# Kernel optimization log

Measured on AMD Instinct MI355X. Metric: run time of the kernel, lower is better.

The kernel has to match this reference:

```python
import jax, jax.numpy as jnp
import numpy as np
import math

N_HEAD = 16

def _rope_tables(seq, dh, dtype):
    inv_freq = 1.0 / (10000.0 ** (jnp.arange(0, dh, 2, dtype=jnp.float32) / dh))
    angle = jnp.arange(seq, dtype=jnp.float32)[:, None] * inv_freq[None, :]  # [S, dh/2]
    sin = jnp.repeat(jnp.sin(angle), 2, axis=-1).astype(dtype)  # [S, dh]
    cos = jnp.repeat(jnp.cos(angle), 2, axis=-1).astype(dtype)
    return sin, cos

def _rotate_half(x):
    x_even = x[..., ::2]
    x_odd = x[..., 1::2]
    return jnp.stack([-x_odd, x_even], axis=-1).reshape(x.shape)

def _apply_rope(x, sin, cos):
    # x: [B, H, S, dh]; sin/cos: [S, dh]
    return x * cos[None, None] + _rotate_half(x) * sin[None, None]

def setup_inputs() -> dict:
    key = jax.random.key(0)
    ks = jax.random.split(key, 9)
    B, S, D = 2, 2048, 2048
    scale = 1.0 / math.sqrt(D)
    x = jax.random.normal(ks[0], (B, S, D), dtype=jnp.float32)
    wq = jax.random.normal(ks[1], (D, D), dtype=jnp.float32) * scale
    wk = jax.random.normal(ks[2], (D, D), dtype=jnp.float32) * scale
    wv = jax.random.normal(ks[3], (D, D), dtype=jnp.float32) * scale
    wo = jax.random.normal(ks[4], (D, D), dtype=jnp.float32) * scale
    bq = jnp.zeros((D,), jnp.float32)
    bk = jnp.zeros((D,), jnp.float32)
    bv = jnp.zeros((D,), jnp.float32)
    bo = jnp.zeros((D,), jnp.float32)
    # causal mask: True = masked (strict upper triangle)
    mask = jnp.triu(jnp.ones((S, S), dtype=bool), k=1)[None, None]  # [1,1,S,S]
    return {"x": x, "wq": wq, "bq": bq, "wk": wk, "bk": bk, "wv": wv, "bv": bv,
            "wo": wo, "bo": bo, "mask": mask}

def reference(x, wq, bq, wk, bk, wv, bv, wo, bo, mask):
    B, S, D = x.shape
    H = N_HEAD
    dh = D // H
    # projections (torch Linear: x @ W.T + b)
    q = (x @ wq.T + bq).reshape(B, S, H, dh).transpose(0, 2, 1, 3)  # [B,H,S,dh]
    k = (x @ wk.T + bk).reshape(B, S, H, dh).transpose(0, 2, 1, 3)
    v = (x @ wv.T + bv).reshape(B, S, H, dh).transpose(0, 2, 1, 3)
    sin, cos = _rope_tables(S, dh, x.dtype)
    q = _apply_rope(q, sin, cos)
    k = _apply_rope(k, sin, cos)
    scores = jnp.einsum('bhqd,bhkd->bhqk', q, k) / math.sqrt(dh)
    scores = jnp.where(mask, -jnp.inf, scores)
    attn = jax.nn.softmax(scores, axis=-1)
    attn = jnp.nan_to_num(attn, nan=0.0)
    out = jnp.einsum('bhqk,bhkd->bhqd', attn, v)  # [B,H,S,dh]
    out = out.transpose(0, 2, 1, 3).reshape(B, S, D)
    return out @ wo.T + bo
```

## Files before the change

kernel.cpp:

```cpp
#include <hip/hip_runtime.h>
#include <math.h>


typedef _Float16 half8 __attribute__((ext_vector_type(8)));
typedef _Float16 half4v __attribute__((ext_vector_type(4)));
typedef float f32x4 __attribute__((ext_vector_type(4)));

__device__ __forceinline__ void gl_lds16(const void* g, void* l) {
  __builtin_amdgcn_global_load_lds(
      (const __attribute__((address_space(1))) unsigned int*)g,
      (__attribute__((address_space(3))) unsigned int*)l, 16, 0, 0);
}

__global__ void cast_f32_f16(const float* __restrict__ src, _Float16* __restrict__ dst, int n4) {
  int i = blockIdx.x * blockDim.x + threadIdx.x;
  if (i >= n4) return;
  float4 v = reinterpret_cast<const float4*>(src)[i];
  half4v o;
  o[0] = (_Float16)v.x; o[1] = (_Float16)v.y; o[2] = (_Float16)v.z; o[3] = (_Float16)v.w;
  reinterpret_cast<half4v*>(dst)[i] = o;
}

__global__ void cast_w(const float* __restrict__ w0, const float* __restrict__ w1,
                       const float* __restrict__ w2, const float* __restrict__ w3,
                       _Float16* __restrict__ wdst) {
  const float* s = blockIdx.y == 0 ? w0 : blockIdx.y == 1 ? w1 : blockIdx.y == 2 ? w2 : w3;
  int i = blockIdx.x * blockDim.x + threadIdx.x;
  float4 v = reinterpret_cast<const float4*>(s)[i];
  half4v o;
  o[0] = (_Float16)v.x; o[1] = (_Float16)v.y; o[2] = (_Float16)v.z; o[3] = (_Float16)v.w;
  reinterpret_cast<half4v*>(wdst)[(size_t)blockIdx.y * 1048576 + i] = o;
}

template <bool OUT_F32>
__global__ __launch_bounds__(256, 2) void gemm_bt(
    const _Float16* __restrict__ A,
    const _Float16* __restrict__ B,
    const float* __restrict__ b0, const float* __restrict__ b1,
    const float* __restrict__ b2,
    void* __restrict__ Cout,
    int M, int N, int K) {
  __shared__ _Float16 As[2][4096];
  __shared__ _Float16 Bs[2][4096];
  const int bm = blockIdx.y * 128, bn = blockIdx.x * 128;
  const int tid = threadIdx.x;
  const int wave = tid >> 6, lane = tid & 63;
  const int quad = lane >> 4, l16 = lane & 15;
  const int hh = wave >> 1, gg = wave & 1;

  const _Float16* gsrc[4];
  int lofs[4];
#pragma unroll
  for (int p = 0; p < 4; ++p) {
    int c = ((p & 1) * 256 + tid) & 511;
    int cl16 = c & 15, cqd = (c >> 4) & 3, ci = (c >> 6) & 3, ch = c >> 8;
    int grow = ch * 64 + ci * 16 + cl16;
    int gcol = cqd * 8;
    gsrc[p] = (p < 2 ? A + (size_t)(bm + grow) * K : B + (size_t)(bn + grow) * K) + gcol;
    lofs[p] = c * 8;
  }

  f32x4 acc[4][4];
#pragma unroll
  for (int i = 0; i < 4; ++i)
#pragma unroll
    for (int n = 0; n < 4; ++n) acc[i][n] = f32x4{0.f, 0.f, 0.f, 0.f};

#pragma unroll
  for (int p = 0; p < 4; ++p)
    gl_lds16(gsrc[p], (p < 2 ? &As[0][lofs[p]] : &Bs[0][lofs[p]]));

  const int nit = K >> 5;
  for (int it = 0; it < nit; ++it) {
    __syncthreads();
    const int cur = it & 1;
    if (it + 1 < nit) {
      const int nxt = cur ^ 1, ko = (it + 1) * 32;
#pragma unroll
      for (int p = 0; p < 4; ++p)
        gl_lds16(gsrc[p] + ko, (p < 2 ? &As[nxt][lofs[p]] : &Bs[nxt][lofs[p]]));
    }
    half8 af[4], bf[4];
#pragma unroll
    for (int i = 0; i < 4; ++i)
      af[i] = *reinterpret_cast<const half8*>(&As[cur][((hh * 4 + i) * 4 + quad) * 128 + l16 * 8]);
#pragma unroll
    for (int n = 0; n < 4; ++n)
      bf[n] = *reinterpret_cast<const half8*>(&Bs[cur][((gg * 4 + n) * 4 + quad) * 128 + l16 * 8]);
#pragma unroll
    for (int i = 0; i < 4; ++i)
#pragma unroll
      for (int n = 0; n < 4; ++n)
        acc[i][n] = __builtin_amdgcn_mfma_f32_16x16x32_f16(af[i], bf[n], acc[i][n], 0, 0, 0);
  }

  const int wm = hh * 64, wn = gg * 64;
#pragma unroll
  for (int n = 0; n < 4; ++n) {
    const int gc = bn + wn + n * 16 + l16;
    const float* bp = (gc < 2048) ? b0 : (gc < 4096 ? b1 : b2);
    const float bz = bp[gc & 2047];
#pragma unroll
    for (int i = 0; i < 4; ++i) {
#pragma unroll
      for (int r = 0; r < 4; ++r) {
        const int gr = bm + wm + i * 16 + quad * 4 + r;
        float v = acc[i][n][r] + bz;
        if (OUT_F32)
          reinterpret_cast<float*>(Cout)[(size_t)gr * N + gc] = v;
        else
          reinterpret_cast<_Float16*>(Cout)[(size_t)gr * N + gc] = (_Float16)v;
      }
    }
  }
}

__global__ void rope_inplace(_Float16* __restrict__ qkv, int ngroups) {
  int idx = blockIdx.x * blockDim.x + threadIdx.x;
  if (idx >= ngroups) return;
  int m = idx >> 8;
  int g = idx & 255;
  int s = m & 2047;
  const float scale = 0.088388347648318447f;
  size_t base = (size_t)m * 6144 + g * 8;
  half8 qv = *reinterpret_cast<const half8*>(qkv + base);
  half8 kv = *reinterpret_cast<const half8*>(qkv + base + 2048);
  half8 qo, ko;
#pragma unroll
  for (int j = 0; j < 4; ++j) {
    int i = (g * 4 + j) & 63;
    float ang = (float)s * exp2f(-0.2076205059304601f * (float)i);
    float sn, cs;
    __sincosf(ang, &sn, &cs);
    float e = (float)qv[j * 2], o = (float)qv[j * 2 + 1];
    qo[j * 2]     = (_Float16)((e * cs - o * sn) * scale);
    qo[j * 2 + 1] = (_Float16)((o * cs + e * sn) * scale);
    e = (float)kv[j * 2]; o = (float)kv[j * 2 + 1];
    ko[j * 2]     = (_Float16)(e * cs - o * sn);
    ko[j * 2 + 1] = (_Float16)(o * cs + e * sn);
  }
  *reinterpret_cast<half8*>(qkv + base) = qo;
  *reinterpret_cast<half8*>(qkv + base + 2048) = ko;
}

__global__ __launch_bounds__(256) void transpose_v(const _Float16* __restrict__ qkv,
                                                   _Float16* __restrict__ vt) {
  __shared__ _Float16 t[64][72];
  const int s0 = blockIdx.x * 64;
  const int d0 = blockIdx.y * 64;
  const int bh = blockIdx.z;
  const int b = bh >> 4, h = bh & 15;
  const int tid = threadIdx.x;
#pragma unroll
  for (int p = 0; p < 2; ++p) {
    int chunk = p * 256 + tid;
    int r = chunk >> 3, c8 = (chunk & 7) * 8;
    *reinterpret_cast<half8*>(&t[r][c8]) = *reinterpret_cast<const half8*>(
        &qkv[(size_t)(b * 2048 + s0 + r) * 6144 + 4096 + h * 128 + d0 + c8]);
  }
  __syncthreads();
#pragma unroll
  for (int p = 0; p < 2; ++p) {
    int chunk = p * 256 + tid;
    int dr = chunk >> 3, c8 = (chunk & 7) * 8;
    half8 o;
#pragma unroll
    for (int j = 0; j < 8; ++j) o[j] = t[c8 + j][dr];
    *reinterpret_cast<half8*>(&vt[(size_t)(bh * 128 + d0 + dr) * 2048 + s0 + c8]) = o;
  }
}

__global__ __launch_bounds__(256, 2) void attn_kernel(
    const _Float16* __restrict__ QKV,
    const _Float16* __restrict__ VT,
    _Float16* __restrict__ ctx) {
  constexpr int LD = 6144, S = 2048;
  __shared__ _Float16 Ks[2][8192];
  __shared__ _Float16 Vs[2][8192];
  __shared__ _Float16 P[4][16][80];
  const int bid = blockIdx.x;
  const int bh = bid & 31;
  const int qt = 31 - (bid >> 5);
  const int b = bh >> 4, h = bh & 15;
  const int tid = threadIdx.x;
  const int wv = tid >> 6, lane = tid & 63;
  const int quad = lane >> 4, l16 = lane & 15;
  const int q0 = qt * 64 + wv * 16;

  const _Float16* qp = QKV + (size_t)(b * S + q0 + l16) * LD + h * 128;
  half8 aq[4];
#pragma unroll
  for (int ks = 0; ks < 4; ++ks)
    aq[ks] = *reinterpret_cast<const half8*>(qp + ks * 32 + quad * 8);

  const _Float16* gk[4];
  const _Float16* gv[4];
  int lofs[4];
#pragma unroll
  for (int p = 0; p < 4; ++p) {
    int c = p * 256 + tid;
    int cl16 = c & 15, cqd = (c >> 4) & 3;
    int cks = (c >> 6) & 3, cf = c >> 8;
    gk[p] = QKV + (size_t)(b * S + cf * 16 + cl16) * LD + 2048 + h * 128 + cks * 32 + cqd * 8;
    int ckv = (c >> 6) & 1, ct = c >> 7;
    gv[p] = VT + (size_t)(bh * 128 + ct * 16 + cl16) * S + ckv * 32 + cqd * 8;
    lofs[p] = c * 8;
  }

  f32x4 acc[8];
#pragma unroll
  for (int t = 0; t < 8; ++t) acc[t] = f32x4{0.f, 0.f, 0.f, 0.f};
  f32x4 lacc = f32x4{0.f, 0.f, 0.f, 0.f};
  float m_i[4];
#pragma unroll
  for (int r = 0; r < 4; ++r) m_i[r] = -INFINITY;

  half8 ones;
#pragma unroll
  for (int j = 0; j < 8; ++j) ones[j] = (_Float16)1.0f;

#pragma unroll
  for (int p = 0; p < 4; ++p) gl_lds16(gk[p], &Ks[0][lofs[p]]);
#pragma unroll
  for (int p = 0; p < 4; ++p) gl_lds16(gv[p], &Vs[0][lofs[p]]);

  for (int j = 0; j <= qt; ++j) {
    __syncthreads();
    const int cur = j & 1;
    if (j < qt) {
      const size_t ko = (size_t)(j + 1) * 64 * LD;
      const int vo = (j + 1) * 64;
#pragma unroll
      for (int p = 0; p < 4; ++p) gl_lds16(gk[p] + ko, &Ks[cur ^ 1][lofs[p]]);
#pragma unroll
      for (int p = 0; p < 4; ++p) gl_lds16(gv[p] + vo, &Vs[cur ^ 1][lofs[p]]);
    }
    f32x4 sf[4];
#pragma unroll
    for (int f = 0; f < 4; ++f) sf[f] = f32x4{0.f, 0.f, 0.f, 0.f};
#pragma unroll
    for (int f = 0; f < 4; ++f)
#pragma unroll
      for (int ks = 0; ks < 4; ++ks) {
        half8 bk = *reinterpret_cast<const half8*>(&Ks[cur][((f * 4 + ks) * 4 + quad) * 128 + l16 * 8]);
        sf[f] = __builtin_amdgcn_mfma_f32_16x16x32_f16(aq[ks], bk, sf[f], 0, 0, 0);
      }
    if (j == qt) {
      const int key0 = j * 64;
#pragma unroll
      for (int f = 0; f < 4; ++f) {
        const int key = key0 + f * 16 + l16;
#pragma unroll
        for (int r = 0; r < 4; ++r) {
          const int row = q0 + quad * 4 + r;
          sf[f][r] = (key <= row) ? sf[f][r] : -1e30f;
        }
      }
    }
    float alpha[4];
#pragma unroll
    for (int r = 0; r < 4; ++r) {
      float tm = fmaxf(fmaxf(sf[0][r], sf[1][r]), fmaxf(sf[2][r], sf[3][r]));
      tm = fmaxf(tm, __shfl_xor(tm, 1));
      tm = fmaxf(tm, __shfl_xor(tm, 2));
      tm = fmaxf(tm, __shfl_xor(tm, 4));
      tm = fmaxf(tm, __shfl_xor(tm, 8));
      const float mn = fmaxf(m_i[r], tm);
      alpha[r] = __expf(m_i[r] - mn);
      m_i[r] = mn;
    }
#pragma unroll
    for (int f = 0; f < 4; ++f)
#pragma unroll
      for (int r = 0; r < 4; ++r)
        P[wv][quad * 4 + r][f * 16 + l16] = (_Float16)__expf(sf[f][r] - m_i[r]);
    half8 pa0 = *reinterpret_cast<const half8*>(&P[wv][l16][quad * 8]);
    half8 pa1 = *reinterpret_cast<const half8*>(&P[wv][l16][32 + quad * 8]);
#pragma unroll
    for (int t = 0; t < 8; ++t)
#pragma unroll
      for (int r = 0; r < 4; ++r) acc[t][r] *= alpha[r];
#pragma unroll
    for (int r = 0; r < 4; ++r) lacc[r] *= alpha[r];
#pragma unroll
    for (int t = 0; t < 8; ++t) {
      half8 bv0 = *reinterpret_cast<const half8*>(&Vs[cur][((t * 2 + 0) * 4 + quad) * 128 + l16 * 8]);
      half8 bv1 = *reinterpret_cast<const half8*>(&Vs[cur][((t * 2 + 1) * 4 + quad) * 128 + l16 * 8]);
      acc[t] = __builtin_amdgcn_mfma_f32_16x16x32_f16(pa0, bv0, acc[t], 0, 0, 0);
      acc[t] = __builtin_amdgcn_mfma_f32_16x16x32_f16(pa1, bv1, acc[t], 0, 0, 0);
    }
    lacc = __builtin_amdgcn_mfma_f32_16x16x32_f16(pa0, ones, lacc, 0, 0, 0);
    lacc = __builtin_amdgcn_mfma_f32_16x16x32_f16(pa1, ones, lacc, 0, 0, 0);
  }

  float inv[4];
#pragma unroll
  for (int r = 0; r < 4; ++r) inv[r] = 1.0f / lacc[r];
#pragma unroll
  for (int t = 0; t < 8; ++t)
#pragma unroll
    for (int r = 0; r < 4; ++r)
      ctx[(size_t)(b * S + q0 + quad * 4 + r) * 2048 + h * 128 + t * 16 + l16] =
          (_Float16)(acc[t][r] * inv[r]);
}

extern "C" void kernel_launch(void* const* d_in, const int* in_sizes, int n_in,
                              void* d_out, int out_size, void* d_ws, size_t ws_size,
                              hipStream_t stream) {
  const float* x  = (const float*)d_in[0];
  const float* wq = (const float*)d_in[1];
  const float* bq = (const float*)d_in[2];
  const float* wk = (const float*)d_in[3];
  const float* bk = (const float*)d_in[4];
  const float* wv = (const float*)d_in[5];
  const float* bv = (const float*)d_in[6];
  const float* wo = (const float*)d_in[7];
  const float* bo = (const float*)d_in[8];

  _Float16* W      = (_Float16*)d_ws;
  _Float16* xh     = W;
  _Float16* wqkvh  = xh + 8388608;
  _Float16* woh    = wqkvh + 12582912;
  _Float16* qkvlin = woh + 4194304;
  _Float16* vT     = xh;
  _Float16* ctx    = wqkvh;

  cast_f32_f16<<<8192, 256, 0, stream>>>(x, xh, 2097152);
  cast_w<<<dim3(4096, 4), 256, 0, stream>>>(wq, wk, wv, wo, wqkvh);

  gemm_bt<false><<<dim3(48, 32), 256, 0, stream>>>(xh, wqkvh, bq, bk, bv, qkvlin,
                                                   4096, 6144, 2048);

  rope_inplace<<<4096, 256, 0, stream>>>(qkvlin, 1048576);
  transpose_v<<<dim3(32, 2, 32), 256, 0, stream>>>(qkvlin, vT);
  attn_kernel<<<1024, 256, 0, stream>>>(qkvlin, vT, ctx);

  gemm_bt<true><<<dim3(16, 32), 256, 0, stream>>>(ctx, woh, bo, bo, bo, (float*)d_out,
                                                  4096, 2048, 2048);
}
```

Measured before the change: 515.0 us.

## Replace 128x128 GEMM with 256x256 tiled, XOR-swizzled, phase-interleaved pipelined kernel

Rewrites the projection GEMM to use 256x256 output tiles with 512 threads, K-steps of 64, an XOR-swizzled LDS layout, and staged global-to-LDS prefetch split into four phases interleaved with MFMA blocks, using s_setprio and explicit vmcnt waits. The goal is higher arithmetic intensity per loaded byte, fewer LDS bank conflicts and better overlap of loads with matrix math. In exchange it uses 128KB of LDS per block and more accumulator registers. The output projection launches only 128 blocks, which may underfill the GPU's 256 CUs.

```diff
diff --git a/kernel.cpp b/kernel.cpp
--- a/kernel.cpp
+++ b/kernel.cpp
@@ -33,79 +33,154 @@
 }
 
 template <bool OUT_F32>
-__global__ __launch_bounds__(256, 2) void gemm_bt(
+__global__ __launch_bounds__(512, 2) void gemm_bt256(
     const _Float16* __restrict__ A,
     const _Float16* __restrict__ B,
     const float* __restrict__ b0, const float* __restrict__ b1,
     const float* __restrict__ b2,
     void* __restrict__ Cout,
     int M, int N, int K) {
-  __shared__ _Float16 As[2][4096];
-  __shared__ _Float16 Bs[2][4096];
-  const int bm = blockIdx.y * 128, bn = blockIdx.x * 128;
+  __shared__ _Float16 As[2][16384];
+  __shared__ _Float16 Bs[2][16384];
+  const int bm = blockIdx.y * 256, bn = blockIdx.x * 256;
   const int tid = threadIdx.x;
   const int wave = tid >> 6, lane = tid & 63;
   const int quad = lane >> 4, l16 = lane & 15;
-  const int hh = wave >> 1, gg = wave & 1;
-
-  const _Float16* gsrc[4];
-  int lofs[4];
-#pragma unroll
-  for (int p = 0; p < 4; ++p) {
-    int c = ((p & 1) * 256 + tid) & 511;
-    int cl16 = c & 15, cqd = (c >> 4) & 3, ci = (c >> 6) & 3, ch = c >> 8;
-    int grow = ch * 64 + ci * 16 + cl16;
-    int gcol = cqd * 8;
-    gsrc[p] = (p < 2 ? A + (size_t)(bm + grow) * K : B + (size_t)(bn + grow) * K) + gcol;
-    lofs[p] = c * 8;
-  }
-
-  f32x4 acc[4][4];
-#pragma unroll
-  for (int i = 0; i < 4; ++i)
-#pragma unroll
-    for (int n = 0; n < 4; ++n) acc[i][n] = f32x4{0.f, 0.f, 0.f, 0.f};
-
-#pragma unroll
-  for (int p = 0; p < 4; ++p)
-    gl_lds16(gsrc[p], (p < 2 ? &As[0][lofs[p]] : &Bs[0][lofs[p]]));
-
-  const int nit = K >> 5;
-  for (int it = 0; it < nit; ++it) {
-    __syncthreads();
-    const int cur = it & 1;
-    if (it + 1 < nit) {
-      const int nxt = cur ^ 1, ko = (it + 1) * 32;
-#pragma unroll
-      for (int p = 0; p < 4; ++p)
-        gl_lds16(gsrc[p] + ko, (p < 2 ? &As[nxt][lofs[p]] : &Bs[nxt][lofs[p]]));
-    }
-    half8 af[4], bf[4];
+  const int wm = (wave >> 2) * 128, wn = (wave & 3) * 64;
+
+  const int srow = tid >> 3;
+  const int sslot = (tid & 7) ^ (srow & 7);
+  const _Float16* Ag = A + (size_t)(bm + srow) * K + sslot * 8;
+  const _Float16* Bg = B + (size_t)(bn + srow) * K + sslot * 8;
+
+#define STAGE_A(buf, h, c, kt)                                      \
+  gl_lds16(Ag + (size_t)((h) * 128 + (c) * 64) * K + (kt) * 64,     \
+           &As[buf][(h) * 8192 + (c) * 4096 + tid * 8])
+#define STAGE_B(buf, h, c, kt)                                      \
+  gl_lds16(Bg + (size_t)((h) * 128 + (c) * 64) * K + (kt) * 64,     \
+           &Bs[buf][(h) * 8192 + (c) * 4096 + tid * 8])
+
+  const int axor = l16 & 7;
+  const int sl0 = ((0 + quad) ^ axor) * 8;
+  const int sl1 = ((4 + quad) ^ axor) * 8;
+  const int aoff = (wm + l16) * 64;
+  const int boff = (wn + l16) * 64;
+
+#define RD_A(i, kk) \
+  (*reinterpret_cast<const half8*>(&As[cur][aoff + (i) * 1024 + ((kk) ? sl1 : sl0)]))
+#define RD_B(j, kk) \
+  (*reinterpret_cast<const half8*>(&Bs[cur][boff + (j) * 1024 + ((kk) ? sl1 : sl0)]))
+
+  f32x4 acc[8][4];
+#pragma unroll
+  for (int i = 0; i < 8; ++i)
+#pragma unroll
+    for (int j = 0; j < 4; ++j) acc[i][j] = f32x4{0.f, 0.f, 0.f, 0.f};
+
+  half8 a[4][2], b[4][2];
+  const int NT = K >> 6;
+
+  STAGE_A(0, 0, 0, 0); STAGE_A(0, 0, 1, 0);
+  STAGE_A(0, 1, 0, 0); STAGE_A(0, 1, 1, 0);
+  STAGE_B(0, 0, 0, 0); STAGE_B(0, 0, 1, 0);
+  STAGE_B(0, 1, 0, 0); STAGE_B(0, 1, 1, 0);
+  if (NT > 1) {
+    STAGE_A(1, 0, 0, 1); STAGE_A(1, 0, 1, 1);
+    asm volatile("s_waitcnt vmcnt(2)");
+  } else {
+    asm volatile("s_waitcnt vmcnt(0)");
+  }
+  __builtin_amdgcn_s_barrier();
+
+  for (int t = 0; t < NT; ++t) {
+    const int cur = t & 1, nxt = cur ^ 1;
+    const bool pf = (t + 1 < NT);
+    const bool pf2 = (t + 2 < NT);
+
+#pragma unroll
+    for (int i = 0; i < 4; ++i) {
+      a[i][0] = RD_A(i, 0); a[i][1] = RD_A(i, 1);
+    }
+#pragma unroll
+    for (int j = 0; j < 2; ++j) {
+      b[j][0] = RD_B(j, 0); b[j][1] = RD_B(j, 1);
+    }
+    if (pf) { STAGE_A(nxt, 1, 0, t + 1); STAGE_A(nxt, 1, 1, t + 1); }
+    __builtin_amdgcn_s_barrier();
+    __builtin_amdgcn_s_setprio(1);
 #pragma unroll
     for (int i = 0; i < 4; ++i)
-      af[i] = *reinterpret_cast<const half8*>(&As[cur][((hh * 4 + i) * 4 + quad) * 128 + l16 * 8]);
-#pragma unroll
-    for (int n = 0; n < 4; ++n)
-      bf[n] = *reinterpret_cast<const half8*>(&Bs[cur][((gg * 4 + n) * 4 + quad) * 128 + l16 * 8]);
+#pragma unroll
+      for (int j = 0; j < 2; ++j) {
+        acc[i][j] = __builtin_amdgcn_mfma_f32_16x16x32_f16(a[i][0], b[j][0], acc[i][j], 0, 0, 0);
+        acc[i][j] = __builtin_amdgcn_mfma_f32_16x16x32_f16(a[i][1], b[j][1], acc[i][j], 0, 0, 0);
+      }
+    __builtin_amdgcn_s_setprio(0);
+    __builtin_amdgcn_s_barrier();
+
+#pragma unroll
+    for (int j = 2; j < 4; ++j) {
+      b[j][0] = RD_B(j, 0); b[j][1] = RD_B(j, 1);
+    }
+    if (pf) { STAGE_B(nxt, 0, 0, t + 1); STAGE_B(nxt, 0, 1, t + 1); }
+    __builtin_amdgcn_s_barrier();
+    __builtin_amdgcn_s_setprio(1);
 #pragma unroll
     for (int i = 0; i < 4; ++i)
 #pragma unroll
-      for (int n = 0; n < 4; ++n)
-        acc[i][n] = __builtin_amdgcn_mfma_f32_16x16x32_f16(af[i], bf[n], acc[i][n], 0, 0, 0);
-  }
-
-  const int wm = hh * 64, wn = gg * 64;
-#pragma unroll
-  for (int n = 0; n < 4; ++n) {
-    const int gc = bn + wn + n * 16 + l16;
+      for (int j = 2; j < 4; ++j) {
+        acc[i][j] = __builtin_amdgcn_mfma_f32_16x16x32_f16(a[i][0], b[j][0], acc[i][j], 0, 0, 0);
+        acc[i][j] = __builtin_amdgcn_mfma_f32_16x16x32_f16(a[i][1], b[j][1], acc[i][j], 0, 0, 0);
+      }
+    __builtin_amdgcn_s_setprio(0);
+    __builtin_amdgcn_s_barrier();
+
+#pragma unroll
+    for (int i = 0; i < 4; ++i) {
+      a[i][0] = RD_A(i + 4, 0); a[i][1] = RD_A(i + 4, 1);
+    }
+    if (pf) { STAGE_B(nxt, 1, 0, t + 1); STAGE_B(nxt, 1, 1, t + 1); }
+    __builtin_amdgcn_s_barrier();
+    __builtin_amdgcn_s_setprio(1);
+#pragma unroll
+    for (int i = 0; i < 4; ++i)
+#pragma unroll
+      for (int j = 0; j < 2; ++j) {
+        acc[i + 4][j] = __builtin_amdgcn_mfma_f32_16x16x32_f16(a[i][0], b[j][0], acc[i + 4][j], 0, 0, 0);
+        acc[i + 4][j] = __builtin_amdgcn_mfma_f32_16x16x32_f16(a[i][1], b[j][1], acc[i + 4][j], 0, 0, 0);
+      }
+    __builtin_amdgcn_s_setprio(0);
+    __builtin_amdgcn_s_barrier();
+
+    if (pf2) { STAGE_A(cur, 0, 0, t + 2); STAGE_A(cur, 0, 1, t + 2); }
+    __builtin_amdgcn_s_barrier();
+    __builtin_amdgcn_s_setprio(1);
+#pragma unroll
+    for (int i = 0; i < 4; ++i)
+#pragma unroll
+      for (int j = 2; j < 4; ++j) {
+        acc[i + 4][j] = __builtin_amdgcn_mfma_f32_16x16x32_f16(a[i][0], b[j][0], acc[i + 4][j], 0, 0, 0);
+        acc[i + 4][j] = __builtin_amdgcn_mfma_f32_16x16x32_f16(a[i][1], b[j][1], acc[i + 4][j], 0, 0, 0);
+      }
+    __builtin_amdgcn_s_setprio(0);
+    if (pf2)
+      asm volatile("s_waitcnt vmcnt(2)");
+    else
+      asm volatile("s_waitcnt vmcnt(0)");
+    __builtin_amdgcn_s_barrier();
+  }
+
+#pragma unroll
+  for (int j = 0; j < 4; ++j) {
+    const int gc = bn + wn + j * 16 + l16;
     const float* bp = (gc < 2048) ? b0 : (gc < 4096 ? b1 : b2);
     const float bz = bp[gc & 2047];
 #pragma unroll
-    for (int i = 0; i < 4; ++i) {
+    for (int i = 0; i < 8; ++i) {
 #pragma unroll
       for (int r = 0; r < 4; ++r) {
         const int gr = bm + wm + i * 16 + quad * 4 + r;
-        float v = acc[i][n][r] + bz;
+        float v = acc[i][j][r] + bz;
         if (OUT_F32)
           reinterpret_cast<float*>(Cout)[(size_t)gr * N + gc] = v;
         else
@@ -113,6 +188,10 @@
       }
     }
   }
+#undef STAGE_A
+#undef STAGE_B
+#undef RD_A
+#undef RD_B
 }
 
 __global__ void rope_inplace(_Float16* __restrict__ qkv, int ngroups) {
@@ -328,13 +407,13 @@
   cast_f32_f16<<<8192, 256, 0, stream>>>(x, xh, 2097152);
   cast_w<<<dim3(4096, 4), 256, 0, stream>>>(wq, wk, wv, wo, wqkvh);
 
-  gemm_bt<false><<<dim3(48, 32), 256, 0, stream>>>(xh, wqkvh, bq, bk, bv, qkvlin,
-                                                   4096, 6144, 2048);
+  gemm_bt256<false><<<dim3(24, 16), 512, 0, stream>>>(xh, wqkvh, bq, bk, bv, qkvlin,
+                                                      4096, 6144, 2048);
 
   rope_inplace<<<4096, 256, 0, stream>>>(qkvlin, 1048576);
   transpose_v<<<dim3(32, 2, 32), 256, 0, stream>>>(qkvlin, vT);
   attn_kernel<<<1024, 256, 0, stream>>>(qkvlin, vT, ctx);
 
-  gemm_bt<true><<<dim3(16, 32), 256, 0, stream>>>(ctx, woh, bo, bo, bo, (float*)d_out,
-                                                  4096, 2048, 2048);
-}
+  gemm_bt256<true><<<dim3(8, 16), 512, 0, stream>>>(ctx, woh, bo, bo, bo, (float*)d_out,
+                                                    4096, 2048, 2048);
+}
```

New measurement: 452.9 us. 1.14x faster.
